# Performance work log

Hardware: AMD Instinct MI355X
Metric: run time of the kernel (lower is better)

## Reference

```python
import math
import jax, jax.numpy as jnp
import numpy as np

B, L, D, H = 256, 32, 512, 512
NEG_INF = -1e9


def setup_inputs() -> dict:
    key = jax.random.key(0)
    ks = jax.random.split(key, 7)
    x = jax.random.normal(ks[0], (B, L, D), dtype=jnp.float32)
    length = jax.random.randint(ks[1], (B,), 2, L + 1)  # valid lengths in [2, L]
    # word_linear: D -> 2H
    W_word = jax.random.normal(ks[2], (2 * H, D), dtype=jnp.float32) * (1.0 / math.sqrt(D))
    b_word = jnp.zeros((2 * H,), dtype=jnp.float32)
    # comp_linear: 2H -> 5H (orthogonal-ish init; scale is fine for a reference)
    W_comp = jax.random.normal(ks[3], (5 * H, 2 * H), dtype=jnp.float32) * (1.0 / math.sqrt(2 * H))
    b_comp = jnp.zeros((5 * H,), dtype=jnp.float32)
    comp_query = jax.random.normal(ks[4], (H,), dtype=jnp.float32) * 0.01
    return {"x": x, "length": length, "W_word": W_word, "b_word": b_word,
            "W_comp": W_comp, "b_comp": b_comp, "comp_query": comp_query}


def _treelstm_compose(hl, cl, hr, cr, W_comp, b_comp):
    # hl/hr: [B, n, H] -> parent h, c: [B, n, H]
    v = jnp.einsum('bnd,kd->bnk', jnp.concatenate([hl, hr], axis=2), W_comp) + b_comp
    i, fl, fr, u, o = jnp.split(v, 5, axis=2)
    c = cl * jax.nn.sigmoid(fl + 1.0) + cr * jax.nn.sigmoid(fr + 1.0) \
        + jnp.tanh(u) * jax.nn.sigmoid(i)
    h = jax.nn.sigmoid(o) * jnp.tanh(c)
    return h, c


def reference(x, length, W_word, b_word, W_comp, b_comp, comp_query):
    length_mask = (jnp.arange(L)[None, :] < length[:, None]).astype(jnp.float32)  # [B, L]
    # leaf states from word_linear (use_leaf_rnn=False path)
    hc = jnp.einsum('bld,kd->blk', x, W_word) + b_word  # [B, L, 2H]
    h, c = jnp.split(hc, 2, axis=2)
    scale = 1.0 / math.sqrt(H)
    for i in range(L - 1):
        new_h, new_c = _treelstm_compose(h[:, :-1], c[:, :-1], h[:, 1:], c[:, 1:], W_comp, b_comp)
        if i < L - 2:
            # eval-mode greedy composition selection (basic.greedy_select)
            logits = jnp.sum(comp_query * new_h, axis=-1) * scale  # [B, L-1-i]
            mask = length_mask[:, i + 1:]
            logits = jnp.where(mask > 0, logits, NEG_INF)
            select = jax.nn.one_hot(jnp.argmax(logits, axis=1), logits.shape[1], dtype=jnp.float32)
            cum = jnp.cumsum(select, axis=1)
            left = (1.0 - cum)[:, :, None]
            right = (cum - select)[:, :, None]
            sel = select[:, :, None]
            new_h = sel * new_h + left * h[:, :-1] + right * h[:, 1:]
            new_c = sel * new_c + left * c[:, :-1] + right * c[:, 1:]
        done = length_mask[:, i + 1][:, None, None]
        h = done * new_h + (1.0 - done) * h[:, :-1]
        c = done * new_c + (1.0 - done) * c[:, :-1]
    return h[:, 0, :]  # final root hidden state [B, H]
```

## Files before the change

### kernel.cpp

```cpp
#include <hip/hip_runtime.h>
#include <cmath>

#define B_   256
#define L_   32
#define H_   512
#define NH5  2560
#define N2   5120
#define SCALE 0.044194173824159216f

__device__ float g_h [B_*L_*H_];
__device__ float g_c [B_*L_*H_];
__device__ float g_al[(size_t)B_*L_*NH5];
__device__ float g_ar[(size_t)B_*L_*NH5];
__device__ float g_logit[B_*L_];
__device__ int   g_list[B_*L_];
__device__ int   g_count[B_];
__device__ int   g_merged[B_];
__device__ int   g_mpos[B_];
__device__ int   g_rows[B_*L_];
__device__ int   g_nrows;
__device__ int   g_mlist[2][B_];
__device__ int   g_cnt[2];

__device__ __forceinline__ float sigm(float x) { return 1.0f / (1.0f + expf(-x)); }

__device__ __forceinline__ void gate4(float* d, const float* __restrict__ a,
                                      const float* __restrict__ b,
                                      const float* __restrict__ bc, int off) {
  float4 x = *(const float4*)(a + off);
  float4 y = *(const float4*)(b + off);
  float4 z = *(const float4*)(bc + off);
  d[0]=x.x+y.x+z.x; d[1]=x.y+y.y+z.y; d[2]=x.z+y.z+z.z; d[3]=x.w+y.w+z.w;
}
__device__ __forceinline__ void gate2(float* d, const float* __restrict__ a,
                                      const float* __restrict__ b,
                                      const float* __restrict__ bc, int off) {
  float2 x = *(const float2*)(a + off);
  float2 y = *(const float2*)(b + off);
  float2 z = *(const float2*)(bc + off);
  d[0]=x.x+y.x+z.x; d[1]=x.y+y.y+z.y;
}

__global__ __launch_bounds__(256) void scan_init(const int* __restrict__ length) {
  __shared__ int sw[4];
  __shared__ int s_off[256];
  __shared__ int s_len[256];
  const int t = threadIdx.x;
  const int len = length[t];
  s_len[t] = len;
  int v = len;
#pragma unroll
  for (int off = 1; off < 64; off <<= 1) {
    int o = __shfl_up(v, off, 64);
    if ((t & 63) >= off) v += o;
  }
  if ((t & 63) == 63) sw[t >> 6] = v;
  __syncthreads();
  int base = 0;
  for (int w = 0; w < (t >> 6); w++) base += sw[w];
  const int incl = base + v;
  s_off[t] = incl - len;
  if (t == 255) g_nrows = incl;
  g_count[t] = len; g_merged[t] = -2; g_mpos[t] = 0;
  if (t == 0) { g_cnt[0] = 0; g_cnt[1] = 0; }
  __syncthreads();
  for (int idx = t; idx < B_*L_; idx += 256) {
    const int b = idx >> 5, s = idx & 31;
    g_list[idx] = s;
    if (s < s_len[b]) g_rows[s_off[b] + s] = idx;
  }
}

template<int MODE>
__global__ __launch_bounds__(256) void gemm_big(
    const float* __restrict__ Aext,
    const float* __restrict__ Bm,
    const float* __restrict__ bias)
{
  const int NR = g_nrows;
  const int m0 = blockIdx.y * 128;
  if (m0 >= NR) return;
  const int n0 = blockIdx.x * 128;

  const int tid = threadIdx.x;
  const int w = tid >> 6, l = tid & 63;
  const int tx = (w & 1) * 8 + (l & 7);
  const int ty = (w >> 1) * 8 + (l >> 3);

  __shared__ float As[2][8][128];
  __shared__ float Bs[2][8][128];

  const int ra = tid >> 1, qa = (tid & 1) * 4;

  const float* Abase = (MODE == 0) ? Aext : g_h;
  int mr = m0 + ra; if (mr >= NR) mr = NR - 1;
  const float* aptr = Abase + (size_t)g_rows[mr] * 512 + qa;

  const float* bptr;
  {
    int nrow = n0 + ra;
    if (MODE == 0) bptr = Bm + (size_t)nrow * 512 + qa;
    else bptr = Bm + (nrow < NH5 ? (size_t)nrow * 1024
                                 : (size_t)(nrow - NH5) * 1024 + 512) + qa;
  }

  float4 av = *(const float4*)(aptr);
  float4 bv = *(const float4*)(bptr);
  As[0][qa+0][ra]=av.x; As[0][qa+1][ra]=av.y; As[0][qa+2][ra]=av.z; As[0][qa+3][ra]=av.w;
  Bs[0][qa+0][ra]=bv.x; Bs[0][qa+1][ra]=bv.y; Bs[0][qa+2][ra]=bv.z; Bs[0][qa+3][ra]=bv.w;
  __syncthreads();

  float acc[8][8] = {};

  for (int s = 0; s < 64; ++s) {
    const int cur = s & 1;
    if (s < 63) {
      av = *(const float4*)(aptr + 8*(s+1));
      bv = *(const float4*)(bptr + 8*(s+1));
    }
#pragma unroll
    for (int k = 0; k < 8; k++) {
      float af[8], bf[8];
#pragma unroll
      for (int c = 0; c < 2; c++) {
        float4 t = *(const float4*)&As[cur][k][ty*8 + 4*c];
        af[4*c+0]=t.x; af[4*c+1]=t.y; af[4*c+2]=t.z; af[4*c+3]=t.w;
      }
#pragma unroll
      for (int c = 0; c < 2; c++) {
        float4 t = *(const float4*)&Bs[cur][k][tx*8 + 4*c];
        bf[4*c+0]=t.x; bf[4*c+1]=t.y; bf[4*c+2]=t.z; bf[4*c+3]=t.w;
      }
#pragma unroll
      for (int i = 0; i < 8; i++)
#pragma unroll
        for (int j = 0; j < 8; j++)
          acc[i][j] = fmaf(af[i], bf[j], acc[i][j]);
    }
    if (s < 63) {
      const int nx = cur ^ 1;
      As[nx][qa+0][ra]=av.x; As[nx][qa+1][ra]=av.y; As[nx][qa+2][ra]=av.z; As[nx][qa+3][ra]=av.w;
      Bs[nx][qa+0][ra]=bv.x; Bs[nx][qa+1][ra]=bv.y; Bs[nx][qa+2][ra]=bv.z; Bs[nx][qa+3][ra]=bv.w;
      __syncthreads();
    }
  }

#pragma unroll
  for (int i = 0; i < 8; i++) {
    int mrow = m0 + ty*8 + i;
    if (mrow >= NR) continue;
    int crow = g_rows[mrow];
#pragma unroll
    for (int jc = 0; jc < 2; jc++) {
      int n = n0 + tx*8 + jc*4;
      float4 v = make_float4(acc[i][jc*4+0], acc[i][jc*4+1],
                             acc[i][jc*4+2], acc[i][jc*4+3]);
      if (MODE == 0) {
        float4 b4 = *(const float4*)(bias + n);
        v.x += b4.x; v.y += b4.y; v.z += b4.z; v.w += b4.w;
        if (n < H_) *(float4*)(g_h + (size_t)crow*H_ + n)        = v;
        else        *(float4*)(g_c + (size_t)crow*H_ + (n - H_)) = v;
      } else {
        if (n < NH5) *(float4*)(g_al + (size_t)crow*NH5 + n)         = v;
        else         *(float4*)(g_ar + (size_t)crow*NH5 + (n - NH5)) = v;
      }
    }
  }
}

__global__ __launch_bounds__(256) void iter0_logits(const int* __restrict__ length,
                                                    const float* __restrict__ bc,
                                                    const float* __restrict__ qv) {
  __shared__ float sred[4];
  const int p = blockIdx.x, b = blockIdx.y;
  if (p >= length[b] - 1) return;
  const float* al = g_al + (size_t)(b*L_ + p)*NH5;
  const float* ar = g_ar + (size_t)(b*L_ + p + 1)*NH5;
  const float* cl = g_c  + (size_t)(b*L_ + p)*H_;
  const float* cr = g_c  + (size_t)(b*L_ + p + 1)*H_;
  const int j0 = threadIdx.x * 2;
  float vi[2], vfl[2], vfr[2], vu[2], vo[2];
  gate2(vi , al, ar, bc,        j0);
  gate2(vfl, al, ar, bc, H_   + j0);
  gate2(vfr, al, ar, bc, 2*H_ + j0);
  gate2(vu , al, ar, bc, 3*H_ + j0);
  gate2(vo , al, ar, bc, 4*H_ + j0);
  float2 CL = *(const float2*)(cl + j0);
  float2 CR = *(const float2*)(cr + j0);
  float2 Q  = *(const float2*)(qv + j0);
  const float clv[2] = {CL.x, CL.y};
  const float crv[2] = {CR.x, CR.y};
  const float qq [2] = {Q.x, Q.y};
  float part = 0.f;
#pragma unroll
  for (int u = 0; u < 2; ++u) {
    float c = clv[u]*sigm(vfl[u]+1.f) + crv[u]*sigm(vfr[u]+1.f) + tanhf(vu[u])*sigm(vi[u]);
    float h = sigm(vo[u])*tanhf(c);
    part = fmaf(qq[u], h, part);
  }
#pragma unroll
  for (int off = 32; off; off >>= 1) part += __shfl_down(part, off, 64);
  if ((threadIdx.x & 63) == 0) sred[threadIdx.x >> 6] = part;
  __syncthreads();
  if (threadIdx.x == 0)
    g_logit[b*L_ + p] = (sred[0]+sred[1]+sred[2]+sred[3]) * SCALE;
}

__global__ __launch_bounds__(256) void select_merge(int iter,
    const int* __restrict__ length,
    const float* __restrict__ bc,
    const float* __restrict__ qv,
    float* __restrict__ out)
{
  __shared__ float sred[4];
  __shared__ int s_sel[3];
  const int b = blockIdx.x, tid = threadIdx.x;
  const bool fin = (iter == L_-2);
  if (b == 0 && tid == 0) g_cnt[(iter & 1) ^ 1] = 0;

  const int m     = g_count[b];
  const int pslot = g_merged[b];
  const int ppos  = g_mpos[b];
  int* list = g_list + b*L_;

  if (iter > 0 && pslot >= 0) {
    const int half = tid >> 7, lt = tid & 127;
    int sl = -1, sr = -1;
    if (half == 0) { if (ppos > 0)     { sl = list[ppos-1]; sr = list[ppos];   } }
    else           { if (ppos < m - 1) { sl = list[ppos];   sr = list[ppos+1]; } }
    float part = 0.f;
    if (sl >= 0) {
      const float* al = g_al + (size_t)(b*L_+sl)*NH5;
      const float* ar = g_ar + (size_t)(b*L_+sr)*NH5;
      const float* cl = g_c  + (size_t)(b*L_+sl)*H_;
      const float* cr = g_c  + (size_t)(b*L_+sr)*H_;
      const int j0 = lt * 4;
      float vi[4], vfl[4], vfr[4], vu[4], vo[4];
      gate4(vi , al, ar, bc,        j0);
      gate4(vfl, al, ar, bc, H_   + j0);
      gate4(vfr, al, ar, bc, 2*H_ + j0);
      gate4(vu , al, ar, bc, 3*H_ + j0);
      gate4(vo , al, ar, bc, 4*H_ + j0);
      float4 CL = *(const float4*)(cl + j0);
      float4 CR = *(const float4*)(cr + j0);
      float4 Q  = *(const float4*)(qv + j0);
      const float clv[4] = {CL.x,CL.y,CL.z,CL.w};
      const float crv[4] = {CR.x,CR.y,CR.z,CR.w};
      const float qq [4] = {Q.x,Q.y,Q.z,Q.w};
#pragma unroll
      for (int u = 0; u < 4; ++u) {
        float c = clv[u]*sigm(vfl[u]+1.f) + crv[u]*sigm(vfr[u]+1.f) + tanhf(vu[u])*sigm(vi[u]);
        float h = sigm(vo[u])*tanhf(c);
        part = fmaf(qq[u], h, part);
      }
    }
#pragma unroll
    for (int off = 32; off; off >>= 1) part += __shfl_down(part, off, 64);
    if ((tid & 63) == 0) sred[tid >> 6] = part;
    __syncthreads();
    if (tid == 0   && ppos > 0)     g_logit[b*L_ + list[ppos-1]] = (sred[0]+sred[1])*SCALE;
    if (tid == 128 && ppos < m - 1) g_logit[b*L_ + list[ppos]]   = (sred[2]+sred[3])*SCALE;
  }

  const bool active = iter < (length[b] - 1);
  if (!active) {
    if (tid == 0) g_merged[b] = -1;
    if (fin) {
      const float* hr = g_h + (size_t)(b*L_)*H_;
      const int j0 = tid * 2;
      *(float2*)(out + (size_t)b*H_ + j0) = *(const float2*)(hr + j0);
    }
    return;
  }

  __syncthreads();

  if (tid < 64) {
    float lg = -1e30f; int idx = tid;
    if (tid < m - 1) lg = g_logit[b*L_ + list[tid]];
#pragma unroll
    for (int off = 32; off; off >>= 1) {
      float olg = __shfl_down(lg, off, 64);
      int   oid = __shfl_down(idx, off, 64);
      if (olg > lg || (olg == lg && oid < idx)) { lg = olg; idx = oid; }
    }
    if (tid == 0) { s_sel[0] = idx; s_sel[1] = list[idx]; s_sel[2] = list[idx+1]; }
  }
  __syncthreads();
  const int pos = s_sel[0], sl = s_sel[1], sr = s_sel[2];

  {
    const float* al = g_al + (size_t)(b*L_+sl)*NH5;
    const float* ar = g_ar + (size_t)(b*L_+sr)*NH5;
    float*       cl = g_c  + (size_t)(b*L_+sl)*H_;
    const float* cr = g_c  + (size_t)(b*L_+sr)*H_;
    float*       hl = g_h  + (size_t)(b*L_+sl)*H_;
    const int j0 = tid * 2;
    float vi[2], vfl[2], vfr[2], vu[2], vo[2];
    gate2(vi , al, ar, bc,        j0);
    gate2(vfl, al, ar, bc, H_   + j0);
    gate2(vfr, al, ar, bc, 2*H_ + j0);
    gate2(vu , al, ar, bc, 3*H_ + j0);
    gate2(vo , al, ar, bc, 4*H_ + j0);
    float2 CL = *(const float2*)(cl + j0);
    float2 CR = *(const float2*)(cr + j0);
    const float clv[2] = {CL.x, CL.y};
    const float crv[2] = {CR.x, CR.y};
    float cc[2], hh[2];
#pragma unroll
    for (int u = 0; u < 2; ++u) {
      float c = clv[u]*sigm(vfl[u]+1.f) + crv[u]*sigm(vfr[u]+1.f) + tanhf(vu[u])*sigm(vi[u]);
      cc[u] = c; hh[u] = sigm(vo[u])*tanhf(c);
    }
    *(float2*)(cl + j0) = make_float2(cc[0], cc[1]);
    *(float2*)(hl + j0) = make_float2(hh[0], hh[1]);
    if (fin)
      *(float2*)(out + (size_t)b*H_ + j0) = make_float2(hh[0], hh[1]);
  }
  if (tid == 0) {
    for (int n = pos+1; n < m-1; n++) list[n] = list[n+1];
    g_count[b]  = m - 1;
    g_merged[b] = sl;
    g_mpos[b]   = pos;
    int k = atomicAdd(&g_cnt[iter & 1], 1);
    g_mlist[iter & 1][k] = b;
  }
}

__global__ __launch_bounds__(256) void gemm_iter(int par, const float* __restrict__ Wc)
{
  const int nact = g_cnt[par];
  const int m0 = blockIdx.y * 32;
  if (m0 >= nact) return;
  const int n0 = blockIdx.x * 64;
  const int tid = threadIdx.x;

  __shared__ float As[2][32][32];
  __shared__ float Bs[2][32][64];

  const int ra = tid >> 3, qa = (tid & 7) * 4;
  int mr = m0 + ra; if (mr >= nact) mr = nact - 1;
  const int bbA = g_mlist[par][mr];
  const float* aptr = g_h + (size_t)(bbA*L_ + g_merged[bbA]) * 512 + qa;

  const int rb = tid >> 2, qb = (tid & 3) * 8;
  const int nr = n0 + rb;
  const float* bptr = (nr < NH5) ? Wc + (size_t)nr * 1024 + qb
                                 : Wc + (size_t)(nr - NH5) * 1024 + 512 + qb;

  const int tx = tid & 15, ty = tid >> 4;

  float4 av  = *(const float4*)(aptr);
  float4 bv0 = *(const float4*)(bptr);
  float4 bv1 = *(const float4*)(bptr + 4);
  As[0][qa+0][ra]=av.x;  As[0][qa+1][ra]=av.y;  As[0][qa+2][ra]=av.z;  As[0][qa+3][ra]=av.w;
  Bs[0][qb+0][rb]=bv0.x; Bs[0][qb+1][rb]=bv0.y; Bs[0][qb+2][rb]=bv0.z; Bs[0][qb+3][rb]=bv0.w;
  Bs[0][qb+4][rb]=bv1.x; Bs[0][qb+5][rb]=bv1.y; Bs[0][qb+6][rb]=bv1.z; Bs[0][qb+7][rb]=bv1.w;
  __syncthreads();

  float acc[2][4] = {};
  for (int s = 0; s < 16; ++s) {
    const int cur = s & 1;
    if (s < 15) {
      const int ko = 32 * (s + 1);
      av  = *(const float4*)(aptr + ko);
      bv0 = *(const float4*)(bptr + ko);
      bv1 = *(const float4*)(bptr + ko + 4);
    }
#pragma unroll
    for (int k = 0; k < 32; k++) {
      float2 a2 = *(const float2*)&As[cur][k][ty*2];
      float4 b4 = *(const float4*)&Bs[cur][k][tx*4];
      acc[0][0] = fmaf(a2.x, b4.x, acc[0][0]);
      acc[0][1] = fmaf(a2.x, b4.y, acc[0][1]);
      acc[0][2] = fmaf(a2.x, b4.z, acc[0][2]);
      acc[0][3] = fmaf(a2.x, b4.w, acc[0][3]);
      acc[1][0] = fmaf(a2.y, b4.x, acc[1][0]);
      acc[1][1] = fmaf(a2.y, b4.y, acc[1][1]);
      acc[1][2] = fmaf(a2.y, b4.z, acc[1][2]);
      acc[1][3] = fmaf(a2.y, b4.w, acc[1][3]);
    }
    if (s < 15) {
      const int nx = cur ^ 1;
      As[nx][qa+0][ra]=av.x;  As[nx][qa+1][ra]=av.y;  As[nx][qa+2][ra]=av.z;  As[nx][qa+3][ra]=av.w;
      Bs[nx][qb+0][rb]=bv0.x; Bs[nx][qb+1][rb]=bv0.y; Bs[nx][qb+2][rb]=bv0.z; Bs[nx][qb+3][rb]=bv0.w;
      Bs[nx][qb+4][rb]=bv1.x; Bs[nx][qb+5][rb]=bv1.y; Bs[nx][qb+6][rb]=bv1.z; Bs[nx][qb+7][rb]=bv1.w;
      __syncthreads();
    }
  }

#pragma unroll
  for (int i = 0; i < 2; i++) {
    int mrow = m0 + ty*2 + i;
    if (mrow >= nact) continue;
    int bb = g_mlist[par][mrow];
    size_t base = (size_t)(bb*L_ + g_merged[bb]) * NH5;
    int n = n0 + tx*4;
    float4 v = make_float4(acc[i][0], acc[i][1], acc[i][2], acc[i][3]);
    if (n < NH5) *(float4*)(g_al + base + n)         = v;
    else         *(float4*)(g_ar + base + (n - NH5)) = v;
  }
}

extern "C" void kernel_launch(void* const* d_in, const int* in_sizes, int n_in,
                              void* d_out, int out_size, void* d_ws, size_t ws_size,
                              hipStream_t stream)
{
  (void)in_sizes; (void)n_in; (void)out_size; (void)d_ws; (void)ws_size;
  const float* x      = (const float*)d_in[0];
  const int*   length = (const int*)  d_in[1];
  const float* W_word = (const float*)d_in[2];
  const float* b_word = (const float*)d_in[3];
  const float* W_comp = (const float*)d_in[4];
  const float* b_comp = (const float*)d_in[5];
  const float* q      = (const float*)d_in[6];
  float* out = (float*)d_out;

  scan_init<<<1, 256, 0, stream>>>(length);

  gemm_big<0><<<dim3(1024/128, 64), 256, 0, stream>>>(x, W_word, b_word);
  gemm_big<1><<<dim3(N2/128,   64), 256, 0, stream>>>(nullptr, W_comp, nullptr);

  iter0_logits<<<dim3(L_-1, B_), 256, 0, stream>>>(length, b_comp, q);

  for (int i = 0; i < L_-1; i++) {
    select_merge<<<B_, 256, 0, stream>>>(i, length, b_comp, q, out);
    if (i < L_-2)
      gemm_iter<<<dim3(N2/64, 8), 256, 0, stream>>>(i & 1, W_comp);
  }
}
```

Before: 1.596 ms.

## Enlarge gemm_iter M tile to 64 rows and single-buffer gemm_big shared memory

gemm_iter now computes a 64x64 output tile per block with a 4x4 register micro-tile instead of 32x64 with 2x4. Each block reads W_comp once per 64 active rows instead of once per 32, which halves weight reads per iteration, and the grid's M dimension shrinks from 8 to 4. gemm_big drops its shared-memory double buffer in favour of a single buffer with two barriers per K step, and its epilogue switches from float4 to scalar stores. The gemm_big changes reduce LDS use but add barriers and narrower stores, which may cost throughput in the large one-time GEMMs.

After: 1.662 ms. 1.04x slower.

```diff
diff --git a/kernel.cpp b/kernel.cpp
--- a/kernel.cpp
+++ b/kernel.cpp
@@ -87,8 +87,8 @@
   const int tx = (w & 1) * 8 + (l & 7);
   const int ty = (w >> 1) * 8 + (l >> 3);
 
-  __shared__ float As[2][8][128];
-  __shared__ float Bs[2][8][128];
+  __shared__ float As[8][128];
+  __shared__ float Bs[8][128];
 
   const int ra = tid >> 1, qa = (tid & 1) * 4;
 
@@ -106,29 +106,28 @@
 
   float4 av = *(const float4*)(aptr);
   float4 bv = *(const float4*)(bptr);
-  As[0][qa+0][ra]=av.x; As[0][qa+1][ra]=av.y; As[0][qa+2][ra]=av.z; As[0][qa+3][ra]=av.w;
-  Bs[0][qa+0][ra]=bv.x; Bs[0][qa+1][ra]=bv.y; Bs[0][qa+2][ra]=bv.z; Bs[0][qa+3][ra]=bv.w;
-  __syncthreads();
-
   float acc[8][8] = {};
 
-  for (int s = 0; s < 64; ++s) {
-    const int cur = s & 1;
-    if (s < 63) {
-      av = *(const float4*)(aptr + 8*(s+1));
-      bv = *(const float4*)(bptr + 8*(s+1));
+  for (int k0 = 0; k0 < 512; k0 += 8) {
+    __syncthreads();
+    As[qa+0][ra] = av.x; As[qa+1][ra] = av.y; As[qa+2][ra] = av.z; As[qa+3][ra] = av.w;
+    Bs[qa+0][ra] = bv.x; Bs[qa+1][ra] = bv.y; Bs[qa+2][ra] = bv.z; Bs[qa+3][ra] = bv.w;
+    __syncthreads();
+    if (k0 + 8 < 512) {
+      av = *(const float4*)(aptr + k0 + 8);
+      bv = *(const float4*)(bptr + k0 + 8);
     }
 #pragma unroll
     for (int k = 0; k < 8; k++) {
       float af[8], bf[8];
 #pragma unroll
       for (int c = 0; c < 2; c++) {
-        float4 t = *(const float4*)&As[cur][k][ty*8 + 4*c];
+        float4 t = *(const float4*)&As[k][ty*8 + 4*c];
         af[4*c+0]=t.x; af[4*c+1]=t.y; af[4*c+2]=t.z; af[4*c+3]=t.w;
       }
 #pragma unroll
       for (int c = 0; c < 2; c++) {
-        float4 t = *(const float4*)&Bs[cur][k][tx*8 + 4*c];
+        float4 t = *(const float4*)&Bs[k][tx*8 + 4*c];
         bf[4*c+0]=t.x; bf[4*c+1]=t.y; bf[4*c+2]=t.z; bf[4*c+3]=t.w;
       }
 #pragma unroll
@@ -136,12 +135,6 @@
 #pragma unroll
         for (int j = 0; j < 8; j++)
           acc[i][j] = fmaf(af[i], bf[j], acc[i][j]);
-    }
-    if (s < 63) {
-      const int nx = cur ^ 1;
-      As[nx][qa+0][ra]=av.x; As[nx][qa+1][ra]=av.y; As[nx][qa+2][ra]=av.z; As[nx][qa+3][ra]=av.w;
-      Bs[nx][qa+0][ra]=bv.x; Bs[nx][qa+1][ra]=bv.y; Bs[nx][qa+2][ra]=bv.z; Bs[nx][qa+3][ra]=bv.w;
-      __syncthreads();
     }
   }
 
@@ -151,18 +144,16 @@
     if (mrow >= NR) continue;
     int crow = g_rows[mrow];
 #pragma unroll
-    for (int jc = 0; jc < 2; jc++) {
-      int n = n0 + tx*8 + jc*4;
-      float4 v = make_float4(acc[i][jc*4+0], acc[i][jc*4+1],
-                             acc[i][jc*4+2], acc[i][jc*4+3]);
+    for (int j = 0; j < 8; j++) {
+      int n = n0 + tx*8 + j;
+      float v = acc[i][j];
       if (MODE == 0) {
-        float4 b4 = *(const float4*)(bias + n);
-        v.x += b4.x; v.y += b4.y; v.z += b4.z; v.w += b4.w;
-        if (n < H_) *(float4*)(g_h + (size_t)crow*H_ + n)        = v;
-        else        *(float4*)(g_c + (size_t)crow*H_ + (n - H_)) = v;
+        v += bias[n];
+        if (n < H_) g_h[(size_t)crow*H_ + n]        = v;
+        else        g_c[(size_t)crow*H_ + (n - H_)] = v;
       } else {
-        if (n < NH5) *(float4*)(g_al + (size_t)crow*NH5 + n)         = v;
-        else         *(float4*)(g_ar + (size_t)crow*NH5 + (n - NH5)) = v;
+        if (n < NH5) g_al[(size_t)crow*NH5 + n]         = v;
+        else         g_ar[(size_t)crow*NH5 + (n - NH5)] = v;
       }
     }
   }
@@ -330,68 +321,67 @@
 __global__ __launch_bounds__(256) void gemm_iter(int par, const float* __restrict__ Wc)
 {
   const int nact = g_cnt[par];
-  const int m0 = blockIdx.y * 32;
+  const int m0 = blockIdx.y * 64;
   if (m0 >= nact) return;
   const int n0 = blockIdx.x * 64;
   const int tid = threadIdx.x;
 
-  __shared__ float As[2][32][32];
+  __shared__ float As[2][32][64];
   __shared__ float Bs[2][32][64];
 
-  const int ra = tid >> 3, qa = (tid & 7) * 4;
-  int mr = m0 + ra; if (mr >= nact) mr = nact - 1;
+  const int rs = tid >> 2, qs = (tid & 3) * 8;
+  int mr = m0 + rs; if (mr >= nact) mr = nact - 1;
   const int bbA = g_mlist[par][mr];
-  const float* aptr = g_h + (size_t)(bbA*L_ + g_merged[bbA]) * 512 + qa;
-
-  const int rb = tid >> 2, qb = (tid & 3) * 8;
-  const int nr = n0 + rb;
-  const float* bptr = (nr < NH5) ? Wc + (size_t)nr * 1024 + qb
-                                 : Wc + (size_t)(nr - NH5) * 1024 + 512 + qb;
+  const float* aptr = g_h + (size_t)(bbA*L_ + g_merged[bbA]) * 512 + qs;
+
+  const int nr = n0 + rs;
+  const float* bptr = (nr < NH5) ? Wc + (size_t)nr * 1024 + qs
+                                 : Wc + (size_t)(nr - NH5) * 1024 + 512 + qs;
 
   const int tx = tid & 15, ty = tid >> 4;
 
-  float4 av  = *(const float4*)(aptr);
-  float4 bv0 = *(const float4*)(bptr);
-  float4 bv1 = *(const float4*)(bptr + 4);
-  As[0][qa+0][ra]=av.x;  As[0][qa+1][ra]=av.y;  As[0][qa+2][ra]=av.z;  As[0][qa+3][ra]=av.w;
-  Bs[0][qb+0][rb]=bv0.x; Bs[0][qb+1][rb]=bv0.y; Bs[0][qb+2][rb]=bv0.z; Bs[0][qb+3][rb]=bv0.w;
-  Bs[0][qb+4][rb]=bv1.x; Bs[0][qb+5][rb]=bv1.y; Bs[0][qb+6][rb]=bv1.z; Bs[0][qb+7][rb]=bv1.w;
-  __syncthreads();
-
-  float acc[2][4] = {};
+  float4 av0 = *(const float4*)(aptr),  av1 = *(const float4*)(aptr + 4);
+  float4 bv0 = *(const float4*)(bptr),  bv1 = *(const float4*)(bptr + 4);
+  As[0][qs+0][rs]=av0.x; As[0][qs+1][rs]=av0.y; As[0][qs+2][rs]=av0.z; As[0][qs+3][rs]=av0.w;
+  As[0][qs+4][rs]=av1.x; As[0][qs+5][rs]=av1.y; As[0][qs+6][rs]=av1.z; As[0][qs+7][rs]=av1.w;
+  Bs[0][qs+0][rs]=bv0.x; Bs[0][qs+1][rs]=bv0.y; Bs[0][qs+2][rs]=bv0.z; Bs[0][qs+3][rs]=bv0.w;
+  Bs[0][qs+4][rs]=bv1.x; Bs[0][qs+5][rs]=bv1.y; Bs[0][qs+6][rs]=bv1.z; Bs[0][qs+7][rs]=bv1.w;
+  __syncthreads();
+
+  float acc[4][4] = {};
   for (int s = 0; s < 16; ++s) {
     const int cur = s & 1;
     if (s < 15) {
       const int ko = 32 * (s + 1);
-      av  = *(const float4*)(aptr + ko);
-      bv0 = *(const float4*)(bptr + ko);
-      bv1 = *(const float4*)(bptr + ko + 4);
+      av0 = *(const float4*)(aptr + ko);  av1 = *(const float4*)(aptr + ko + 4);
+      bv0 = *(const float4*)(bptr + ko);  bv1 = *(const float4*)(bptr + ko + 4);
     }
 #pragma unroll
     for (int k = 0; k < 32; k++) {
-      float2 a2 = *(const float2*)&As[cur][k][ty*2];
+      float4 a4 = *(const float4*)&As[cur][k][ty*4];
       float4 b4 = *(const float4*)&Bs[cur][k][tx*4];
-      acc[0][0] = fmaf(a2.x, b4.x, acc[0][0]);
-      acc[0][1] = fmaf(a2.x, b4.y, acc[0][1]);
-      acc[0][2] = fmaf(a2.x, b4.z, acc[0][2]);
-      acc[0][3] = fmaf(a2.x, b4.w, acc[0][3]);
-      acc[1][0] = fmaf(a2.y, b4.x, acc[1][0]);
-      acc[1][1] = fmaf(a2.y, b4.y, acc[1][1]);
-      acc[1][2] = fmaf(a2.y, b4.z, acc[1][2]);
-      acc[1][3] = fmaf(a2.y, b4.w, acc[1][3]);
+      acc[0][0]=fmaf(a4.x,b4.x,acc[0][0]); acc[0][1]=fmaf(a4.x,b4.y,acc[0][1]);
+      acc[0][2]=fmaf(a4.x,b4.z,acc[0][2]); acc[0][3]=fmaf(a4.x,b4.w,acc[0][3]);
+      acc[1][0]=fmaf(a4.y,b4.x,acc[1][0]); acc[1][1]=fmaf(a4.y,b4.y,acc[1][1]);
+      acc[1][2]=fmaf(a4.y,b4.z,acc[1][2]); acc[1][3]=fmaf(a4.y,b4.w,acc[1][3]);
+      acc[2][0]=fmaf(a4.z,b4.x,acc[2][0]); acc[2][1]=fmaf(a4.z,b4.y,acc[2][1]);
+      acc[2][2]=fmaf(a4.z,b4.z,acc[2][2]); acc[2][3]=fmaf(a4.z,b4.w,acc[2][3]);
+      acc[3][0]=fmaf(a4.w,b4.x,acc[3][0]); acc[3][1]=fmaf(a4.w,b4.y,acc[3][1]);
+      acc[3][2]=fmaf(a4.w,b4.z,acc[3][2]); acc[3][3]=fmaf(a4.w,b4.w,acc[3][3]);
     }
     if (s < 15) {
       const int nx = cur ^ 1;
-      As[nx][qa+0][ra]=av.x;  As[nx][qa+1][ra]=av.y;  As[nx][qa+2][ra]=av.z;  As[nx][qa+3][ra]=av.w;
-      Bs[nx][qb+0][rb]=bv0.x; Bs[nx][qb+1][rb]=bv0.y; Bs[nx][qb+2][rb]=bv0.z; Bs[nx][qb+3][rb]=bv0.w;
-      Bs[nx][qb+4][rb]=bv1.x; Bs[nx][qb+5][rb]=bv1.y; Bs[nx][qb+6][rb]=bv1.z; Bs[nx][qb+7][rb]=bv1.w;
+      As[nx][qs+0][rs]=av0.x; As[nx][qs+1][rs]=av0.y; As[nx][qs+2][rs]=av0.z; As[nx][qs+3][rs]=av0.w;
+      As[nx][qs+4][rs]=av1.x; As[nx][qs+5][rs]=av1.y; As[nx][qs+6][rs]=av1.z; As[nx][qs+7][rs]=av1.w;
+      Bs[nx][qs+0][rs]=bv0.x; Bs[nx][qs+1][rs]=bv0.y; Bs[nx][qs+2][rs]=bv0.z; Bs[nx][qs+3][rs]=bv0.w;
+      Bs[nx][qs+4][rs]=bv1.x; Bs[nx][qs+5][rs]=bv1.y; Bs[nx][qs+6][rs]=bv1.z; Bs[nx][qs+7][rs]=bv1.w;
       __syncthreads();
     }
   }
 
 #pragma unroll
-  for (int i = 0; i < 2; i++) {
-    int mrow = m0 + ty*2 + i;
+  for (int i = 0; i < 4; i++) {
+    int mrow = m0 + ty*4 + i;
     if (mrow >= nact) continue;
     int bb = g_mlist[par][mrow];
     size_t base = (size_t)(bb*L_ + g_merged[bb]) * NH5;
@@ -426,6 +416,6 @@
   for (int i = 0; i < L_-1; i++) {
     select_merge<<<B_, 256, 0, stream>>>(i, length, b_comp, q, out);
     if (i < L_-2)
-      gemm_iter<<<dim3(N2/64, 8), 256, 0, stream>>>(i & 1, W_comp);
-  }
-}
+      gemm_iter<<<dim3(N2/64, 4), 256, 0, stream>>>(i & 1, W_comp);
+  }
+}
```

## Use 512-thread blocks in the big GEMM and select/merge kernels

Applied to the files above, without the earlier changes.

The big GEMM now runs 512 threads per block, each owning a 4x8 output micro-tile instead of 8x8. Half the threads stage A and the other half stage B, into a single shared buffer guarded by two barriers per k-step, replacing the double-buffered scheme. The epilogue now writes scalar stores instead of float4. select_merge also moves to 512 threads with one hidden element per thread, and the neighbour-logit section is adjusted so the extra half does nothing. The intent is lower register pressure and higher occupancy, at the cost of losing load/compute overlap, extra barriers and less coalesced, non-vector stores.

After: 1.624 ms. No clear change (+1.8%).

```diff
diff --git a/kernel.cpp b/kernel.cpp
--- a/kernel.cpp
+++ b/kernel.cpp
@@ -72,7 +72,7 @@
 }
 
 template<int MODE>
-__global__ __launch_bounds__(256) void gemm_big(
+__global__ __launch_bounds__(512) void gemm_big(
     const float* __restrict__ Aext,
     const float* __restrict__ Bm,
     const float* __restrict__ bias)
@@ -83,86 +83,73 @@
   const int n0 = blockIdx.x * 128;
 
   const int tid = threadIdx.x;
-  const int w = tid >> 6, l = tid & 63;
-  const int tx = (w & 1) * 8 + (l & 7);
-  const int ty = (w >> 1) * 8 + (l >> 3);
-
-  __shared__ float As[2][8][128];
-  __shared__ float Bs[2][8][128];
-
-  const int ra = tid >> 1, qa = (tid & 1) * 4;
+  const int tx = tid & 15;
+  const int ty = tid >> 4;
+
+  __shared__ float As[8][128];
+  __shared__ float Bs[8][128];
+
+  const bool stgB = tid >= 256;
+  const int st = tid & 255;
+  const int rs = st >> 1, qs = (st & 1) * 4;
 
   const float* Abase = (MODE == 0) ? Aext : g_h;
-  int mr = m0 + ra; if (mr >= NR) mr = NR - 1;
-  const float* aptr = Abase + (size_t)g_rows[mr] * 512 + qa;
-
-  const float* bptr;
-  {
-    int nrow = n0 + ra;
-    if (MODE == 0) bptr = Bm + (size_t)nrow * 512 + qa;
-    else bptr = Bm + (nrow < NH5 ? (size_t)nrow * 1024
-                                 : (size_t)(nrow - NH5) * 1024 + 512) + qa;
-  }
-
-  float4 av = *(const float4*)(aptr);
-  float4 bv = *(const float4*)(bptr);
-  As[0][qa+0][ra]=av.x; As[0][qa+1][ra]=av.y; As[0][qa+2][ra]=av.z; As[0][qa+3][ra]=av.w;
-  Bs[0][qa+0][ra]=bv.x; Bs[0][qa+1][ra]=bv.y; Bs[0][qa+2][ra]=bv.z; Bs[0][qa+3][ra]=bv.w;
-  __syncthreads();
-
-  float acc[8][8] = {};
-
-  for (int s = 0; s < 64; ++s) {
-    const int cur = s & 1;
-    if (s < 63) {
-      av = *(const float4*)(aptr + 8*(s+1));
-      bv = *(const float4*)(bptr + 8*(s+1));
-    }
+  const float* sptr;
+  if (!stgB) {
+    int mr = m0 + rs; if (mr >= NR) mr = NR - 1;
+    sptr = Abase + (size_t)g_rows[mr] * 512 + qs;
+  } else {
+    int nrow = n0 + rs;
+    if (MODE == 0) sptr = Bm + (size_t)nrow * 512 + qs;
+    else sptr = Bm + (nrow < NH5 ? (size_t)nrow * 1024
+                                 : (size_t)(nrow - NH5) * 1024 + 512) + qs;
+  }
+
+  float4 sv = *(const float4*)(sptr);
+  float acc[4][8] = {};
+
+  for (int k0 = 0; k0 < 512; k0 += 8) {
+    __syncthreads();
+    if (!stgB) {
+      As[qs+0][rs] = sv.x; As[qs+1][rs] = sv.y; As[qs+2][rs] = sv.z; As[qs+3][rs] = sv.w;
+    } else {
+      Bs[qs+0][rs] = sv.x; Bs[qs+1][rs] = sv.y; Bs[qs+2][rs] = sv.z; Bs[qs+3][rs] = sv.w;
+    }
+    __syncthreads();
+    if (k0 + 8 < 512) sv = *(const float4*)(sptr + k0 + 8);
 #pragma unroll
     for (int k = 0; k < 8; k++) {
-      float af[8], bf[8];
-#pragma unroll
-      for (int c = 0; c < 2; c++) {
-        float4 t = *(const float4*)&As[cur][k][ty*8 + 4*c];
-        af[4*c+0]=t.x; af[4*c+1]=t.y; af[4*c+2]=t.z; af[4*c+3]=t.w;
-      }
-#pragma unroll
-      for (int c = 0; c < 2; c++) {
-        float4 t = *(const float4*)&Bs[cur][k][tx*8 + 4*c];
-        bf[4*c+0]=t.x; bf[4*c+1]=t.y; bf[4*c+2]=t.z; bf[4*c+3]=t.w;
-      }
-#pragma unroll
-      for (int i = 0; i < 8; i++)
+      float4 a4 = *(const float4*)&As[k][ty*4];
+      float af[4] = {a4.x, a4.y, a4.z, a4.w};
+      float bf[8];
+      float4 t0 = *(const float4*)&Bs[k][tx*8];
+      float4 t1 = *(const float4*)&Bs[k][tx*8 + 4];
+      bf[0]=t0.x; bf[1]=t0.y; bf[2]=t0.z; bf[3]=t0.w;
+      bf[4]=t1.x; bf[5]=t1.y; bf[6]=t1.z; bf[7]=t1.w;
+#pragma unroll
+      for (int i = 0; i < 4; i++)
 #pragma unroll
         for (int j = 0; j < 8; j++)
           acc[i][j] = fmaf(af[i], bf[j], acc[i][j]);
     }
-    if (s < 63) {
-      const int nx = cur ^ 1;
-      As[nx][qa+0][ra]=av.x; As[nx][qa+1][ra]=av.y; As[nx][qa+2][ra]=av.z; As[nx][qa+3][ra]=av.w;
-      Bs[nx][qa+0][ra]=bv.x; Bs[nx][qa+1][ra]=bv.y; Bs[nx][qa+2][ra]=bv.z; Bs[nx][qa+3][ra]=bv.w;
-      __syncthreads();
-    }
-  }
-
-#pragma unroll
-  for (int i = 0; i < 8; i++) {
-    int mrow = m0 + ty*8 + i;
+  }
+
+#pragma unroll
+  for (int i = 0; i < 4; i++) {
+    int mrow = m0 + ty*4 + i;
     if (mrow >= NR) continue;
     int crow = g_rows[mrow];
 #pragma unroll
-    for (int jc = 0; jc < 2; jc++) {
-      int n = n0 + tx*8 + jc*4;
-      float4 v = make_float4(acc[i][jc*4+0], acc[i][jc*4+1],
-                             acc[i][jc*4+2], acc[i][jc*4+3]);
+    for (int j = 0; j < 8; j++) {
+      int n = n0 + tx*8 + j;
+      float v = acc[i][j];
       if (MODE == 0) {
-        float4 b4 = *(const float4*)(bias + n);
-        v.x += b4.x; v.y += b4.y; v.z += b4.z; v.w += b4.w;
-        if (n < H_) *(float4*)(g_h + (size_t)crow*H_ + n)        = v;
-        else        *(float4*)(g_c + (size_t)crow*H_ + (n - H_)) = v;
+        v += bias[n];
+        if (n < H_) g_h[(size_t)crow*H_ + n]        = v;
+        else        g_c[(size_t)crow*H_ + (n - H_)] = v;
       } else {
-        if (n < NH5) *(float4*)(g_al + (size_t)crow*NH5 + n)         = v;
-        else         *(float4*)(g_ar + (size_t)crow*NH5 + (n - NH5)) = v;
+        if (n < NH5) g_al[(size_t)crow*NH5 + n]         = v;
+        else         g_ar[(size_t)crow*NH5 + (n - NH5)] = v;
       }
     }
   }
@@ -206,7 +193,7 @@
     g_logit[b*L_ + p] = (sred[0]+sred[1]+sred[2]+sred[3]) * SCALE;
 }
 
-__global__ __launch_bounds__(256) void select_merge(int iter,
+__global__ __launch_bounds__(512) void select_merge(int iter,
     const int* __restrict__ length,
     const float* __restrict__ bc,
     const float* __restrict__ qv,
@@ -226,8 +213,8 @@
   if (iter > 0 && pslot >= 0) {
     const int half = tid >> 7, lt = tid & 127;
     int sl = -1, sr = -1;
-    if (half == 0) { if (ppos > 0)     { sl = list[ppos-1]; sr = list[ppos];   } }
-    else           { if (ppos < m - 1) { sl = list[ppos];   sr = list[ppos+1]; } }
+    if (half == 0)      { if (ppos > 0)     { sl = list[ppos-1]; sr = list[ppos];   } }
+    else if (half == 1) { if (ppos < m - 1) { sl = list[ppos];   sr = list[ppos+1]; } }
     float part = 0.f;
     if (sl >= 0) {
       const float* al = g_al + (size_t)(b*L_+sl)*NH5;
@@ -256,7 +243,7 @@
     }
 #pragma unroll
     for (int off = 32; off; off >>= 1) part += __shfl_down(part, off, 64);
-    if ((tid & 63) == 0) sred[tid >> 6] = part;
+    if ((tid & 63) == 0 && tid < 256) sred[tid >> 6] = part;
     __syncthreads();
     if (tid == 0   && ppos > 0)     g_logit[b*L_ + list[ppos-1]] = (sred[0]+sred[1])*SCALE;
     if (tid == 128 && ppos < m - 1) g_logit[b*L_ + list[ppos]]   = (sred[2]+sred[3])*SCALE;
@@ -265,11 +252,8 @@
   const bool active = iter < (length[b] - 1);
   if (!active) {
     if (tid == 0) g_merged[b] = -1;
-    if (fin) {
-      const float* hr = g_h + (size_t)(b*L_)*H_;
-      const int j0 = tid * 2;
-      *(float2*)(out + (size_t)b*H_ + j0) = *(const float2*)(hr + j0);
-    }
+    if (fin)
+      out[(size_t)b*H_ + tid] = g_h[(size_t)(b*L_)*H_ + tid];
     return;
   }
 
@@ -295,27 +279,17 @@
     float*       cl = g_c  + (size_t)(b*L_+sl)*H_;
     const float* cr = g_c  + (size_t)(b*L_+sr)*H_;
     float*       hl = g_h  + (size_t)(b*L_+sl)*H_;
-    const int j0 = tid * 2;
-    float vi[2], vfl[2], vfr[2], vu[2], vo[2];
-    gate2(vi , al, ar, bc,        j0);
-    gate2(vfl, al, ar, bc, H_   + j0);
-    gate2(vfr, al, ar, bc, 2*H_ + j0);
-    gate2(vu , al, ar, bc, 3*H_ + j0);
-    gate2(vo , al, ar, bc, 4*H_ + j0);
-    float2 CL = *(const float2*)(cl + j0);
-    float2 CR = *(const float2*)(cr + j0);
-    const float clv[2] = {CL.x, CL.y};
-    const float crv[2] = {CR.x, CR.y};
-    float cc[2], hh[2];
-#pragma unroll
-    for (int u = 0; u < 2; ++u) {
-      float c = clv[u]*sigm(vfl[u]+1.f) + crv[u]*sigm(vfr[u]+1.f) + tanhf(vu[u])*sigm(vi[u]);
-      cc[u] = c; hh[u] = sigm(vo[u])*tanhf(c);
-    }
-    *(float2*)(cl + j0) = make_float2(cc[0], cc[1]);
-    *(float2*)(hl + j0) = make_float2(hh[0], hh[1]);
+    const int j = tid;
+    float vi  = al[j]       + ar[j]       + bc[j];
+    float vfl = al[H_+j]    + ar[H_+j]    + bc[H_+j];
+    float vfr = al[2*H_+j]  + ar[2*H_+j]  + bc[2*H_+j];
+    float vu  = al[3*H_+j]  + ar[3*H_+j]  + bc[3*H_+j];
+    float vo  = al[4*H_+j]  + ar[4*H_+j]  + bc[4*H_+j];
+    float c = cl[j]*sigm(vfl+1.f) + cr[j]*sigm(vfr+1.f) + tanhf(vu)*sigm(vi);
+    float h = sigm(vo)*tanhf(c);
+    cl[j] = c; hl[j] = h;
     if (fin)
-      *(float2*)(out + (size_t)b*H_ + j0) = make_float2(hh[0], hh[1]);
+      out[(size_t)b*H_ + j] = h;
   }
   if (tid == 0) {
     for (int n = pos+1; n < m-1; n++) list[n] = list[n+1];
@@ -418,13 +392,13 @@
 
   scan_init<<<1, 256, 0, stream>>>(length);
 
-  gemm_big<0><<<dim3(1024/128, 64), 256, 0, stream>>>(x, W_word, b_word);
-  gemm_big<1><<<dim3(N2/128,   64), 256, 0, stream>>>(nullptr, W_comp, nullptr);
+  gemm_big<0><<<dim3(1024/128, 64), 512, 0, stream>>>(x, W_word, b_word);
+  gemm_big<1><<<dim3(N2/128,   64), 512, 0, stream>>>(nullptr, W_comp, nullptr);
 
   iter0_logits<<<dim3(L_-1, B_), 256, 0, stream>>>(length, b_comp, q);
 
   for (int i = 0; i < L_-1; i++) {
-    select_merge<<<B_, 256, 0, stream>>>(i, length, b_comp, q, out);
+    select_merge<<<B_, 512, 0, stream>>>(i, length, b_comp, q, out);
     if (i < L_-2)
       gemm_iter<<<dim3(N2/64, 8), 256, 0, stream>>>(i & 1, W_comp);
   }
```
